# Performance work log

Hardware: AMD Instinct MI355X
Metric: run time of the kernel (lower is better)

Reference implementation:

```python
import jax, jax.numpy as jnp
import numpy as np

B, S, D, U, WIN = 32, 4096, 1024, 1024, 64


def setup_inputs() -> dict:
    key = jax.random.key(0)
    k1, k2, k3, k4, k5 = jax.random.split(key, 5)
    query = jax.random.normal(k1, (B, D), dtype=jnp.float32)
    keys = jax.random.normal(k2, (B, S, D), dtype=jnp.float32)
    key_lengths = jax.random.randint(k3, (B,), S // 2, S).astype(jnp.float32)
    Wq = jax.random.normal(k4, (D, U), dtype=jnp.float32) / np.sqrt(D)
    wp = jax.random.normal(k5, (U, 1), dtype=jnp.float32) / np.sqrt(U)
    return {"query": query, "keys": keys, "key_lengths": key_lengths,
            "Wq": Wq, "wp": wp, "window_size": WIN}


def reference(query, keys, key_lengths, Wq, wp, window_size):
    # dot score: [B,1,D] @ [B,D,S] -> [B,S]
    alignment_score = jnp.einsum('bd,bsd->bs', query, keys)
    weight = jax.nn.softmax(alignment_score, axis=-1)  # F.softmax on 2D -> dim 1

    kl = key_lengths[:, None]                                   # [B,1]
    activated_query = jnp.tanh(query @ Wq)                      # [B,U]
    sigmoid_query = jax.nn.sigmoid(activated_query @ wp)        # [B,1]
    predictive_alignment = kl * sigmoid_query                   # [B,1]

    std2 = jnp.float32((window_size / 2.0) ** 2)
    dist = (kl - predictive_alignment) ** 2                     # [B,1]
    gauss = jnp.exp(-dist / (2.0 * std2))                       # [B,1]

    weight = weight * gauss                                     # [B,S]
    total_context = jnp.einsum('bs,bsd->bd', weight, keys)      # [B,D]
    return total_context, alignment_score
```

## Files before the change

kernel.cpp:

```cpp
#include <hip/hip_runtime.h>
#include <math.h>

#define BB 32
#define SS 4096
#define DD 1024
#define UU 1024
#define TROWS 4
#define CHROWS 256
#define NT (CHROWS / TROWS)
#define CHB (SS / CHROWS)
#define FBLK (BB * CHB)
#define GBLK 128
#define NPART CHB

#define LOAD_LDS16(g, l) __builtin_amdgcn_global_load_lds( \
    (const __attribute__((address_space(1))) unsigned int*)(g), \
    (__attribute__((address_space(3))) unsigned int*)(l), 16, 0, 0)

#define STAGE(ti, dst) do {                                              \
    const char* gt_ = gbase + (size_t)(ti) * 16384;                      \
    char* lb_ = (char*)smem + (dst) * 16384;                             \
    _Pragma("unroll")                                                    \
    for (int j_ = 0; j_ < 4; ++j_)                                       \
        LOAD_LDS16(gt_ + j_ * 4096 + tid * 16, lb_ + j_ * 4096 + tid * 16); \
} while (0)


__global__ __launch_bounds__(256, 3) void fused_kernel(const float* __restrict__ query,
                                                       const float* __restrict__ keys,
                                                       const float* __restrict__ Wq,
                                                       const float* __restrict__ wp,
                                                       float* __restrict__ scores,
                                                       float* __restrict__ mlbuf,
                                                       float* __restrict__ accbuf,
                                                       float* __restrict__ gpart) {
    __shared__ float smem[12288];

    int tid = threadIdx.x;

    if (blockIdx.x < GBLK) {
        int g = blockIdx.x;
        int u0 = g * 8;
        float4* s4 = (float4*)smem;
        for (int i = tid; i < 2048; i += 256) {
            int d = i >> 1, h = i & 1;
            s4[i] = *(const float4*)(Wq + (size_t)d * UU + u0 + h * 4);
        }
        __syncthreads();
        int b = tid >> 3, ui = tid & 7;
        const float* qb = query + (size_t)b * DD;
        float acc = 0.f;
#pragma unroll 8
        for (int d = 0; d < DD; ++d) acc += qb[d] * smem[d * 8 + ui];
        float val = tanhf(acc) * wp[u0 + ui];
        val += __shfl_xor(val, 1, 64);
        val += __shfl_xor(val, 2, 64);
        val += __shfl_xor(val, 4, 64);
        if (ui == 0) gpart[b * GBLK + g] = val;
        return;
    }

    int fb = blockIdx.x - GBLK;
    int b = fb >> 4;
    int chunk = fb & (CHB - 1);
    int s0 = chunk * CHROWS;
    int w = tid >> 6;
    int lane = tid & 63;

    const float4* Q4 = (const float4*)query;
    float4 q0 = Q4[b * 256 + lane],       q1 = Q4[b * 256 + lane + 64],
           q2 = Q4[b * 256 + lane + 128], q3 = Q4[b * 256 + lane + 192];

    const char* gbase = (const char*)(keys + ((size_t)b * SS + s0) * DD);
    float4 a0 = {0,0,0,0}, a1 = {0,0,0,0}, a2 = {0,0,0,0}, a3 = {0,0,0,0};
    float m = -INFINITY, l = 0.f;

    STAGE(0, 0);
    STAGE(1, 1);

    int bf = 0;
    for (int t = 0; t < NT; ++t) {
        if (t + 1 < NT) {
            asm volatile("s_waitcnt vmcnt(4)" ::: "memory");
        } else {
            asm volatile("s_waitcnt vmcnt(0)" ::: "memory");
        }
        __builtin_amdgcn_s_barrier();

        if (t + 2 < NT) {
            int nb = bf + 2; if (nb >= 3) nb -= 3;
            STAGE(t + 2, nb);
        }

        const float* rowp = smem + bf * 4096 + w * 1024;
        float4 k0 = *(const float4*)(rowp + (lane)       * 4);
        float4 k1 = *(const float4*)(rowp + (lane + 64)  * 4);
        float4 k2 = *(const float4*)(rowp + (lane + 128) * 4);
        float4 k3 = *(const float4*)(rowp + (lane + 192) * 4);

        float d = k0.x*q0.x + k0.y*q0.y + k0.z*q0.z + k0.w*q0.w
                + k1.x*q1.x + k1.y*q1.y + k1.z*q1.z + k1.w*q1.w
                + k2.x*q2.x + k2.y*q2.y + k2.z*q2.z + k2.w*q2.w
                + k3.x*q3.x + k3.y*q3.y + k3.z*q3.z + k3.w*q3.w;
#pragma unroll
        for (int o = 32; o > 0; o >>= 1) d += __shfl_xor(d, o, 64);

        if (lane == 0) scores[(size_t)b * SS + s0 + t * TROWS + w] = d;

        float mn = fmaxf(m, d);
        float corr = __expf(m - mn);
        float p = __expf(d - mn);
        l = l * corr + p;
        a0.x = a0.x*corr + p*k0.x; a0.y = a0.y*corr + p*k0.y; a0.z = a0.z*corr + p*k0.z; a0.w = a0.w*corr + p*k0.w;
        a1.x = a1.x*corr + p*k1.x; a1.y = a1.y*corr + p*k1.y; a1.z = a1.z*corr + p*k1.z; a1.w = a1.w*corr + p*k1.w;
        a2.x = a2.x*corr + p*k2.x; a2.y = a2.y*corr + p*k2.y; a2.z = a2.z*corr + p*k2.z; a2.w = a2.w*corr + p*k2.w;
        a3.x = a3.x*corr + p*k3.x; a3.y = a3.y*corr + p*k3.y; a3.z = a3.z*corr + p*k3.z; a3.w = a3.w*corr + p*k3.w;
        m = mn;

        bf += 1; if (bf >= 3) bf -= 3;
    }

    __syncthreads();
    if (lane == 0) { smem[8192 + w] = m; smem[8196 + w] = l; }
    __syncthreads();
    float M = fmaxf(fmaxf(smem[8192], smem[8193]), fmaxf(smem[8194], smem[8195]));
    float Ls = smem[8196] * __expf(smem[8192] - M) + smem[8197] * __expf(smem[8193] - M)
             + smem[8198] * __expf(smem[8194] - M) + smem[8199] * __expf(smem[8195] - M);
    float sw = __expf(m - M);
    float4* aw = (float4*)(smem + (size_t)w * 1024);
    float4 t0 = {a0.x*sw, a0.y*sw, a0.z*sw, a0.w*sw};
    float4 t1 = {a1.x*sw, a1.y*sw, a1.z*sw, a1.w*sw};
    float4 t2 = {a2.x*sw, a2.y*sw, a2.z*sw, a2.w*sw};
    float4 t3 = {a3.x*sw, a3.y*sw, a3.z*sw, a3.w*sw};
    __syncthreads();
    aw[lane] = t0; aw[lane + 64] = t1; aw[lane + 128] = t2; aw[lane + 192] = t3;
    __syncthreads();
    float4 s = {0,0,0,0};
#pragma unroll
    for (int w2 = 0; w2 < 4; ++w2) {
        float4 v = ((const float4*)(smem + (size_t)w2 * 1024))[tid];
        s.x += v.x; s.y += v.y; s.z += v.z; s.w += v.w;
    }
    ((float4*)(accbuf + (size_t)fb * DD))[tid] = s;
    if (tid == 0) { mlbuf[fb * 2] = M; mlbuf[fb * 2 + 1] = Ls; }
}

__global__ void combine_kernel(const float* __restrict__ mlbuf,
                               const float* __restrict__ accbuf,
                               const float* __restrict__ gpart,
                               const float* __restrict__ key_lengths,
                               const int* __restrict__ win,
                               float* __restrict__ ctx) {
    int b = blockIdx.x;
    int d = blockIdx.y * 256 + threadIdx.x;

    __shared__ float red[128];
    __shared__ float mv[NPART], lv[NPART], wexp[NPART];

    if (threadIdx.x < 128) red[threadIdx.x] = gpart[b * GBLK + threadIdx.x];
    if (threadIdx.x < NPART) {
        mv[threadIdx.x] = mlbuf[(b * NPART + threadIdx.x) * 2];
        lv[threadIdx.x] = mlbuf[(b * NPART + threadIdx.x) * 2 + 1];
    }
    __syncthreads();
    for (int t = 64; t > 0; t >>= 1) {
        if (threadIdx.x < t) red[threadIdx.x] += red[threadIdx.x + t];
        __syncthreads();
    }
    float presig = red[0];

    float M = -INFINITY;
#pragma unroll
    for (int i = 0; i < NPART; ++i) M = fmaxf(M, mv[i]);
    float L = 0.f;
#pragma unroll
    for (int i = 0; i < NPART; ++i) L += lv[i] * __expf(mv[i] - M);
    __syncthreads();
    if (threadIdx.x < NPART) wexp[threadIdx.x] = __expf(mv[threadIdx.x] - M);
    __syncthreads();

    float acc = 0.f;
#pragma unroll 8
    for (int i = 0; i < NPART; ++i)
        acc += wexp[i] * accbuf[((size_t)b * NPART + i) * DD + d];

    float sig = 1.f / (1.f + __expf(-presig));
    float kl = key_lengths[b];
    float pa = kl * sig;
    float wv = (float)(*win);
    float std2 = (wv * 0.5f) * (wv * 0.5f);
    float g = __expf(-((kl - pa) * (kl - pa)) / (2.f * std2));

    ctx[(size_t)b * DD + d] = acc * g / L;
}

extern "C" void kernel_launch(void* const* d_in, const int* in_sizes, int n_in,
                              void* d_out, int out_size, void* d_ws, size_t ws_size,
                              hipStream_t stream) {
    const float* query       = (const float*)d_in[0];
    const float* keys        = (const float*)d_in[1];
    const float* key_lengths = (const float*)d_in[2];
    const float* Wq          = (const float*)d_in[3];
    const float* wp          = (const float*)d_in[4];
    const int*   win         = (const int*)d_in[5];

    float* out    = (float*)d_out;
    float* ctx    = out;
    float* scores = out + BB * DD;
    float* wsbuf  = (float*)d_ws;
    float* gpart  = wsbuf;
    float* mlbuf  = wsbuf + 4096;
    float* accbuf = wsbuf + 8192;

    fused_kernel<<<FBLK + GBLK, 256, 0, stream>>>(query, keys, Wq, wp,
                                                  scores, mlbuf, accbuf, gpart);

    dim3 cgrid(BB, DD / 256);
    combine_kernel<<<cgrid, 256, 0, stream>>>(mlbuf, accbuf, gpart, key_lengths, win, ctx);
}
```

Before: 103.1 us.

## Merge combine kernel into fused kernel via cooperative grid sync

Turns the two-kernel sequence into one cooperative launch. After the streaming softmax-accumulate phase, a grid-wide barrier runs, and the first 128 blocks then do the cross-chunk combine and gaussian scaling that the separate combine kernel used to do. This removes the second launch and its gap. In exchange every block must be co-resident (640 blocks at 3 per CU), and grid sync adds a global barrier cost.

```diff
diff --git a/kernel.cpp b/kernel.cpp
--- a/kernel.cpp
+++ b/kernel.cpp
@@ -1,5 +1,8 @@
 #include <hip/hip_runtime.h>
+#include <hip/hip_cooperative_groups.h>
 #include <math.h>
+
+namespace cg = cooperative_groups;
 
 #define BB 32
 #define SS 4096
@@ -30,10 +33,13 @@
                                                        const float* __restrict__ keys,
                                                        const float* __restrict__ Wq,
                                                        const float* __restrict__ wp,
+                                                       const float* __restrict__ key_lengths,
+                                                       const int* __restrict__ win,
                                                        float* __restrict__ scores,
                                                        float* __restrict__ mlbuf,
                                                        float* __restrict__ accbuf,
-                                                       float* __restrict__ gpart) {
+                                                       float* __restrict__ gpart,
+                                                       float* __restrict__ ctx) {
     __shared__ float smem[12288];
 
     int tid = threadIdx.x;
@@ -57,132 +63,128 @@
         val += __shfl_xor(val, 2, 64);
         val += __shfl_xor(val, 4, 64);
         if (ui == 0) gpart[b * GBLK + g] = val;
-        return;
+    } else {
+        int fb = blockIdx.x - GBLK;
+        int b = fb >> 4;
+        int chunk = fb & (CHB - 1);
+        int s0 = chunk * CHROWS;
+        int w = tid >> 6;
+        int lane = tid & 63;
+
+        const float4* Q4 = (const float4*)query;
+        float4 q0 = Q4[b * 256 + lane],       q1 = Q4[b * 256 + lane + 64],
+               q2 = Q4[b * 256 + lane + 128], q3 = Q4[b * 256 + lane + 192];
+
+        const char* gbase = (const char*)(keys + ((size_t)b * SS + s0) * DD);
+        float4 a0 = {0,0,0,0}, a1 = {0,0,0,0}, a2 = {0,0,0,0}, a3 = {0,0,0,0};
+        float m = -INFINITY, l = 0.f;
+
+        STAGE(0, 0);
+        STAGE(1, 1);
+
+        int bf = 0;
+        for (int t = 0; t < NT; ++t) {
+            if (t + 1 < NT) {
+                asm volatile("s_waitcnt vmcnt(4)" ::: "memory");
+            } else {
+                asm volatile("s_waitcnt vmcnt(0)" ::: "memory");
+            }
+            __builtin_amdgcn_s_barrier();
+
+            if (t + 2 < NT) {
+                int nb = bf + 2; if (nb >= 3) nb -= 3;
+                STAGE(t + 2, nb);
+            }
+
+            const float* rowp = smem + bf * 4096 + w * 1024;
+            float4 k0 = *(const float4*)(rowp + (lane)       * 4);
+            float4 k1 = *(const float4*)(rowp + (lane + 64)  * 4);
+            float4 k2 = *(const float4*)(rowp + (lane + 128) * 4);
+            float4 k3 = *(const float4*)(rowp + (lane + 192) * 4);
+
+            float d = k0.x*q0.x + k0.y*q0.y + k0.z*q0.z + k0.w*q0.w
+                    + k1.x*q1.x + k1.y*q1.y + k1.z*q1.z + k1.w*q1.w
+                    + k2.x*q2.x + k2.y*q2.y + k2.z*q2.z + k2.w*q2.w
+                    + k3.x*q3.x + k3.y*q3.y + k3.z*q3.z + k3.w*q3.w;
+#pragma unroll
+            for (int o = 32; o > 0; o >>= 1) d += __shfl_xor(d, o, 64);
+
+            if (lane == 0) scores[(size_t)b * SS + s0 + t * TROWS + w] = d;
+
+            float mn = fmaxf(m, d);
+            float corr = __expf(m - mn);
+            float p = __expf(d - mn);
+            l = l * corr + p;
+            a0.x = a0.x*corr + p*k0.x; a0.y = a0.y*corr + p*k0.y; a0.z = a0.z*corr + p*k0.z; a0.w = a0.w*corr + p*k0.w;
+            a1.x = a1.x*corr + p*k1.x; a1.y = a1.y*corr + p*k1.y; a1.z = a1.z*corr + p*k1.z; a1.w = a1.w*corr + p*k1.w;
+            a2.x = a2.x*corr + p*k2.x; a2.y = a2.y*corr + p*k2.y; a2.z = a2.z*corr + p*k2.z; a2.w = a2.w*corr + p*k2.w;
+            a3.x = a3.x*corr + p*k3.x; a3.y = a3.y*corr + p*k3.y; a3.z = a3.z*corr + p*k3.z; a3.w = a3.w*corr + p*k3.w;
+            m = mn;
+
+            bf += 1; if (bf >= 3) bf -= 3;
+        }
+
+        __syncthreads();
+        if (lane == 0) { smem[8192 + w] = m; smem[8196 + w] = l; }
+        __syncthreads();
+        float M = fmaxf(fmaxf(smem[8192], smem[8193]), fmaxf(smem[8194], smem[8195]));
+        float Ls = smem[8196] * __expf(smem[8192] - M) + smem[8197] * __expf(smem[8193] - M)
+                 + smem[8198] * __expf(smem[8194] - M) + smem[8199] * __expf(smem[8195] - M);
+        float sw = __expf(m - M);
+        float4* aw = (float4*)(smem + (size_t)w * 1024);
+        float4 t0 = {a0.x*sw, a0.y*sw, a0.z*sw, a0.w*sw};
+        float4 t1 = {a1.x*sw, a1.y*sw, a1.z*sw, a1.w*sw};
+        float4 t2 = {a2.x*sw, a2.y*sw, a2.z*sw, a2.w*sw};
+        float4 t3 = {a3.x*sw, a3.y*sw, a3.z*sw, a3.w*sw};
+        __syncthreads();
+        aw[lane] = t0; aw[lane + 64] = t1; aw[lane + 128] = t2; aw[lane + 192] = t3;
+        __syncthreads();
+        float4 s = {0,0,0,0};
+#pragma unroll
+        for (int w2 = 0; w2 < 4; ++w2) {
+            float4 v = ((const float4*)(smem + (size_t)w2 * 1024))[tid];
+            s.x += v.x; s.y += v.y; s.z += v.z; s.w += v.w;
+        }
+        ((float4*)(accbuf + (size_t)fb * DD))[tid] = s;
+        if (tid == 0) { mlbuf[fb * 2] = M; mlbuf[fb * 2 + 1] = Ls; }
     }
 
-    int fb = blockIdx.x - GBLK;
-    int b = fb >> 4;
-    int chunk = fb & (CHB - 1);
-    int s0 = chunk * CHROWS;
-    int w = tid >> 6;
-    int lane = tid & 63;
-
-    const float4* Q4 = (const float4*)query;
-    float4 q0 = Q4[b * 256 + lane],       q1 = Q4[b * 256 + lane + 64],
-           q2 = Q4[b * 256 + lane + 128], q3 = Q4[b * 256 + lane + 192];
-
-    const char* gbase = (const char*)(keys + ((size_t)b * SS + s0) * DD);
-    float4 a0 = {0,0,0,0}, a1 = {0,0,0,0}, a2 = {0,0,0,0}, a3 = {0,0,0,0};
-    float m = -INFINITY, l = 0.f;
-
-    STAGE(0, 0);
-    STAGE(1, 1);
-
-    int bf = 0;
-    for (int t = 0; t < NT; ++t) {
-        if (t + 1 < NT) {
-            asm volatile("s_waitcnt vmcnt(4)" ::: "memory");
-        } else {
-            asm volatile("s_waitcnt vmcnt(0)" ::: "memory");
-        }
-        __builtin_amdgcn_s_barrier();
-
-        if (t + 2 < NT) {
-            int nb = bf + 2; if (nb >= 3) nb -= 3;
-            STAGE(t + 2, nb);
-        }
-
-        const float* rowp = smem + bf * 4096 + w * 1024;
-        float4 k0 = *(const float4*)(rowp + (lane)       * 4);
-        float4 k1 = *(const float4*)(rowp + (lane + 64)  * 4);
-        float4 k2 = *(const float4*)(rowp + (lane + 128) * 4);
-        float4 k3 = *(const float4*)(rowp + (lane + 192) * 4);
-
-        float d = k0.x*q0.x + k0.y*q0.y + k0.z*q0.z + k0.w*q0.w
-                + k1.x*q1.x + k1.y*q1.y + k1.z*q1.z + k1.w*q1.w
-                + k2.x*q2.x + k2.y*q2.y + k2.z*q2.z + k2.w*q2.w
-                + k3.x*q3.x + k3.y*q3.y + k3.z*q3.z + k3.w*q3.w;
-#pragma unroll
-        for (int o = 32; o > 0; o >>= 1) d += __shfl_xor(d, o, 64);
-
-        if (lane == 0) scores[(size_t)b * SS + s0 + t * TROWS + w] = d;
-
-        float mn = fmaxf(m, d);
-        float corr = __expf(m - mn);
-        float p = __expf(d - mn);
-        l = l * corr + p;
-        a0.x = a0.x*corr + p*k0.x; a0.y = a0.y*corr + p*k0.y; a0.z = a0.z*corr + p*k0.z; a0.w = a0.w*corr + p*k0.w;
-        a1.x = a1.x*corr + p*k1.x; a1.y = a1.y*corr + p*k1.y; a1.z = a1.z*corr + p*k1.z; a1.w = a1.w*corr + p*k1.w;
-        a2.x = a2.x*corr + p*k2.x; a2.y = a2.y*corr + p*k2.y; a2.z = a2.z*corr + p*k2.z; a2.w = a2.w*corr + p*k2.w;
-        a3.x = a3.x*corr + p*k3.x; a3.y = a3.y*corr + p*k3.y; a3.z = a3.z*corr + p*k3.z; a3.w = a3.w*corr + p*k3.w;
-        m = mn;
-
-        bf += 1; if (bf >= 3) bf -= 3;
+    cg::this_grid().sync();
+
+    if (blockIdx.x >= GBLK) return;
+    int b = blockIdx.x >> 2;
+    int d = (blockIdx.x & 3) * 256 + tid;
+
+    __shared__ float cred[128];
+    __shared__ float cmv[NPART], clv[NPART], cwexp[NPART];
+    __syncthreads();
+
+    if (tid < 128) cred[tid] = gpart[b * GBLK + tid];
+    if (tid < NPART) {
+        cmv[tid] = mlbuf[(b * NPART + tid) * 2];
+        clv[tid] = mlbuf[(b * NPART + tid) * 2 + 1];
     }
-
-    __syncthreads();
-    if (lane == 0) { smem[8192 + w] = m; smem[8196 + w] = l; }
-    __syncthreads();
-    float M = fmaxf(fmaxf(smem[8192], smem[8193]), fmaxf(smem[8194], smem[8195]));
-    float Ls = smem[8196] * __expf(smem[8192] - M) + smem[8197] * __expf(smem[8193] - M)
-             + smem[8198] * __expf(smem[8194] - M) + smem[8199] * __expf(smem[8195] - M);
-    float sw = __expf(m - M);
-    float4* aw = (float4*)(smem + (size_t)w * 1024);
-    float4 t0 = {a0.x*sw, a0.y*sw, a0.z*sw, a0.w*sw};
-    float4 t1 = {a1.x*sw, a1.y*sw, a1.z*sw, a1.w*sw};
-    float4 t2 = {a2.x*sw, a2.y*sw, a2.z*sw, a2.w*sw};
-    float4 t3 = {a3.x*sw, a3.y*sw, a3.z*sw, a3.w*sw};
-    __syncthreads();
-    aw[lane] = t0; aw[lane + 64] = t1; aw[lane + 128] = t2; aw[lane + 192] = t3;
-    __syncthreads();
-    float4 s = {0,0,0,0};
-#pragma unroll
-    for (int w2 = 0; w2 < 4; ++w2) {
-        float4 v = ((const float4*)(smem + (size_t)w2 * 1024))[tid];
-        s.x += v.x; s.y += v.y; s.z += v.z; s.w += v.w;
+    __syncthreads();
+    for (int t = 64; t > 0; t >>= 1) {
+        if (tid < t) cred[tid] += cred[tid + t];
+        __syncthreads();
     }
-    ((float4*)(accbuf + (size_t)fb * DD))[tid] = s;
-    if (tid == 0) { mlbuf[fb * 2] = M; mlbuf[fb * 2 + 1] = Ls; }
-}
-
-__global__ void combine_kernel(const float* __restrict__ mlbuf,
-                               const float* __restrict__ accbuf,
-                               const float* __restrict__ gpart,
-                               const float* __restrict__ key_lengths,
-                               const int* __restrict__ win,
-                               float* __restrict__ ctx) {
-    int b = blockIdx.x;
-    int d = blockIdx.y * 256 + threadIdx.x;
-
-    __shared__ float red[128];
-    __shared__ float mv[NPART], lv[NPART], wexp[NPART];
-
-    if (threadIdx.x < 128) red[threadIdx.x] = gpart[b * GBLK + threadIdx.x];
-    if (threadIdx.x < NPART) {
-        mv[threadIdx.x] = mlbuf[(b * NPART + threadIdx.x) * 2];
-        lv[threadIdx.x] = mlbuf[(b * NPART + threadIdx.x) * 2 + 1];
-    }
-    __syncthreads();
-    for (int t = 64; t > 0; t >>= 1) {
-        if (threadIdx.x < t) red[threadIdx.x] += red[threadIdx.x + t];
-        __syncthreads();
-    }
-    float presig = red[0];
+    float presig = cred[0];
 
     float M = -INFINITY;
 #pragma unroll
-    for (int i = 0; i < NPART; ++i) M = fmaxf(M, mv[i]);
+    for (int i = 0; i < NPART; ++i) M = fmaxf(M, cmv[i]);
     float L = 0.f;
 #pragma unroll
-    for (int i = 0; i < NPART; ++i) L += lv[i] * __expf(mv[i] - M);
-    __syncthreads();
-    if (threadIdx.x < NPART) wexp[threadIdx.x] = __expf(mv[threadIdx.x] - M);
+    for (int i = 0; i < NPART; ++i) L += clv[i] * __expf(cmv[i] - M);
+    __syncthreads();
+    if (tid < NPART) cwexp[tid] = __expf(cmv[tid] - M);
     __syncthreads();
 
     float acc = 0.f;
 #pragma unroll 8
     for (int i = 0; i < NPART; ++i)
-        acc += wexp[i] * accbuf[((size_t)b * NPART + i) * DD + d];
+        acc += cwexp[i] * accbuf[((size_t)b * NPART + i) * DD + d];
 
     float sig = 1.f / (1.f + __expf(-presig));
     float kl = key_lengths[b];
@@ -212,9 +214,9 @@
     float* mlbuf  = wsbuf + 4096;
     float* accbuf = wsbuf + 8192;
 
-    fused_kernel<<<FBLK + GBLK, 256, 0, stream>>>(query, keys, Wq, wp,
-                                                  scores, mlbuf, accbuf, gpart);
-
-    dim3 cgrid(BB, DD / 256);
-    combine_kernel<<<cgrid, 256, 0, stream>>>(mlbuf, accbuf, gpart, key_lengths, win, ctx);
+    void* args[] = {(void*)&query, (void*)&keys, (void*)&Wq, (void*)&wp,
+                    (void*)&key_lengths, (void*)&win, (void*)&scores,
+                    (void*)&mlbuf, (void*)&accbuf, (void*)&gpart, (void*)&ctx};
+    hipLaunchCooperativeKernel((const void*)fused_kernel,
+                               dim3(FBLK + GBLK), dim3(256), args, 0, stream);
 }
```

Result: slower. 197.6 us (+91.6%).
